# Optimization experiments

Measured on AMD Instinct MI355X. Metric: run time of the kernel, lower is better.

The kernel has to match this reference:

```python
import jax, jax.numpy as jnp
import numpy as np

EMB = 1024  # embedding_size in the torch module


def setup_inputs() -> dict:
    key = jax.random.key(0)
    ks = jax.random.split(key, 6)
    B, N, K = 64, 256, 4096
    y = jax.random.normal(ks[0], (B, N, 1024), dtype=jnp.float32)
    # nn.Linear weights, init normal(std=0.02), zero bias
    Wy_w = jax.random.normal(ks[1], (1024, 1024), dtype=jnp.float32) * 0.02  # [out,in]
    Wy_b = jnp.zeros((1024,), dtype=jnp.float32)
    Wz_w = jax.random.normal(ks[2], (1024, 2048), dtype=jnp.float32) * 0.02  # [out,in]
    Wz_b = jnp.zeros((1024,), dtype=jnp.float32)
    dic_z = jax.random.normal(ks[3], (K, 2048), dtype=jnp.float32)
    prior = jax.random.uniform(ks[4], (K,), dtype=jnp.float32)
    prior = prior / jnp.sum(prior)
    return {"y": y, "Wy_w": Wy_w, "Wy_b": Wy_b, "Wz_w": Wz_w, "Wz_b": Wz_b,
            "dic_z": dic_z, "prior": prior}


def reference(y, Wy_w, Wy_b, Wz_w, Wz_b, dic_z, prior):
    # h = Wy(y): [B,N,1024]; dz = Wz(dic_z): [K,1024]
    h = jnp.einsum('bni,oi->bno', y, Wy_w) + Wy_b
    dz = jnp.einsum('ki,oi->ko', dic_z, Wz_w) + Wz_b
    # attention over dictionary: [B,N,K]
    att = jax.nn.softmax(jnp.einsum('bnd,kd->bnk', h, dz) / jnp.sqrt(jnp.float32(EMB)), axis=-1)
    # z[b,n] = sum_k prior[k] * att[b,n,k] * dic_z[k]  -> [B,N,2048]
    # (avoids the [B,N,K,2048] intermediate the torch code materializes)
    z = jnp.einsum('bnk,k,ke->bne', att, prior, dic_z)
    return z
```

## Files before the change

kernel.cpp:

```cpp
#include <hip/hip_runtime.h>
#include <hip/hip_bf16.h>
#include <stdint.h>

typedef __bf16 bf16;
typedef __bf16 bf16x8 __attribute__((ext_vector_type(8)));
typedef float f32x4 __attribute__((ext_vector_type(4)));
typedef unsigned short ushort8 __attribute__((ext_vector_type(8)));

__device__ __forceinline__ void gload16(const bf16* g, char* l) {
  __builtin_amdgcn_global_load_lds(
      reinterpret_cast<const __attribute__((address_space(1))) unsigned int*>(
          reinterpret_cast<uintptr_t>(g)),
      reinterpret_cast<__attribute__((address_space(3))) unsigned int*>(
          reinterpret_cast<uintptr_t>(l)),
      16, 0, 0);
}

#define VMCNT(n)  asm volatile("s_waitcnt vmcnt(" #n ")" ::: "memory")
#define LGKM0()   do { asm volatile("s_waitcnt lgkmcnt(0)" ::: "memory"); \
                       __builtin_amdgcn_sched_barrier(0); } while (0)
#define BAR()     __builtin_amdgcn_s_barrier()

__global__ __launch_bounds__(256) void cast_bf16(const float* __restrict__ in,
                                                 bf16* __restrict__ out, int n8) {
  int i = blockIdx.x * blockDim.x + threadIdx.x;
  const int stride = gridDim.x * blockDim.x;
  for (; i < n8; i += stride) {
    const float4 v0 = reinterpret_cast<const float4*>(in)[i * 2];
    const float4 v1 = reinterpret_cast<const float4*>(in)[i * 2 + 1];
    bf16x8 o = { (bf16)v0.x, (bf16)v0.y, (bf16)v0.z, (bf16)v0.w,
                 (bf16)v1.x, (bf16)v1.y, (bf16)v1.z, (bf16)v1.w };
    reinterpret_cast<bf16x8*>(out)[i] = o;
  }
}

template <bool OUT_BF16, bool HAS_BIAS, int BN>
__global__ __launch_bounds__(512, 2) void gemm8(
    const bf16* __restrict__ A, const bf16* __restrict__ B,
    const float* __restrict__ bias, void* __restrict__ Cout,
    int M, int N, int K, float scale) {
  constexpr int BUFSZ = 32768 + BN * 128;
  constexpr int BOFF = 32768;
  constexpr int TM = (BN == 256) ? 128 : 64;
  constexpr int MI = TM / 16;
  constexpr int NI = 4;
  constexpr int NPH = MI / 2;
  extern __shared__ char lds[];
  const int tid = threadIdx.x;
  const int lane = tid & 63, w = tid >> 6;

  const int gridN = N / BN;
  const int nwg = gridDim.x;
  const int orig = blockIdx.x;
  int wgid;
  { const int q = nwg >> 3, r = nwg & 7, x = orig & 7, rest = orig >> 3;
    wgid = (x < r ? x * (q + 1) : r * (q + 1) + (x - r) * q) + rest; }
  const int m0 = (wgid / gridN) * 256;
  const int n0 = (wgid % gridN) * BN;

  const int srow = lane >> 3;
  const int scol = ((lane & 7) ^ srow) * 8;
  const bf16* gA = A + (size_t)(m0 + w * 8 + srow) * K + scol;
  const bf16* gB = B + (size_t)(n0 + w * 8 + srow) * K + scol;

  auto stA = [&](char* dst, int u, int h) {
    gload16(gA + (size_t)(h * 128) * K + (size_t)u * 64, dst + h * 16384 + w * 1024);
    gload16(gA + (size_t)(h * 128 + 64) * K + (size_t)u * 64, dst + h * 16384 + 8192 + w * 1024);
  };
  auto stB = [&](char* dst, int u, int h) {
    gload16(gB + (size_t)(h * 128) * K + (size_t)u * 64, dst + BOFF + h * 16384 + w * 1024);
    gload16(gB + (size_t)(h * 128 + 64) * K + (size_t)u * 64, dst + BOFF + h * 16384 + 8192 + w * 1024);
  };

  const int fr = lane & 15, hi = lane >> 4;
  int wm, wn;
  if constexpr (BN == 256) { wm = w >> 2; wn = w & 3; }
  else                     { wm = w >> 1; wn = w & 1; }
  const int abase = (wm * TM + fr) * 128 + ((hi ^ (fr & 7)) << 4);
  const int bbase = BOFF + (wn * 64 + fr) * 128 + ((hi ^ (fr & 7)) << 4);
#define RD_A(b, mi, ks) (*(const bf16x8*)((b) + ((abase + (mi) * 2048) ^ ((ks) << 6))))
#define RD_B(b, ni, ks) (*(const bf16x8*)((b) + ((bbase + (ni) * 2048) ^ ((ks) << 6))))

  f32x4 acc[MI][NI] = {};
  const int NT = K >> 6;

  stA(lds, 0, 0); stA(lds, 0, 1);
  stB(lds, 0, 0);
  if constexpr (BN == 256) stB(lds, 0, 1);
  stB(lds + BUFSZ, 1, 0);
  if constexpr (BN == 256) { stB(lds + BUFSZ, 1, 1); VMCNT(4); }
  else                     { VMCNT(2); }
  BAR();

  for (int u = 0; u < NT; ++u) {
    char* b  = lds + (size_t)(u & 1) * BUFSZ;
    char* bn = lds + (size_t)((u + 1) & 1) * BUFSZ;
    bf16x8 bb[2][NI], a[2][2];
    const bool sA = (u + 1) < NT, sB = (u + 2) < NT;

    if constexpr (BN == 256) {
      a[0][0] = RD_A(b, 0, 0); a[0][1] = RD_A(b, 0, 1);
      a[1][0] = RD_A(b, 1, 0); a[1][1] = RD_A(b, 1, 1);
#pragma unroll
      for (int ni = 0; ni < NI; ++ni) { bb[0][ni] = RD_B(b, ni, 0); bb[1][ni] = RD_B(b, ni, 1); }
      if (sA) stA(bn, u + 1, 0);
      BAR(); LGKM0();
      __builtin_amdgcn_s_setprio(1);
#pragma unroll
      for (int m2 = 0; m2 < 2; ++m2)
#pragma unroll
        for (int ni = 0; ni < NI; ++ni) {
          acc[m2][ni] = __builtin_amdgcn_mfma_f32_16x16x32_bf16(a[m2][0], bb[0][ni], acc[m2][ni], 0, 0, 0);
          acc[m2][ni] = __builtin_amdgcn_mfma_f32_16x16x32_bf16(a[m2][1], bb[1][ni], acc[m2][ni], 0, 0, 0);
        }
      __builtin_amdgcn_s_setprio(0);
      BAR();
      a[0][0] = RD_A(b, 2, 0); a[0][1] = RD_A(b, 2, 1);
      a[1][0] = RD_A(b, 3, 0); a[1][1] = RD_A(b, 3, 1);
      if (sA) stA(bn, u + 1, 1);
      BAR(); LGKM0();
      __builtin_amdgcn_s_setprio(1);
#pragma unroll
      for (int m2 = 0; m2 < 2; ++m2)
#pragma unroll
        for (int ni = 0; ni < NI; ++ni) {
          acc[2 + m2][ni] = __builtin_amdgcn_mfma_f32_16x16x32_bf16(a[m2][0], bb[0][ni], acc[2 + m2][ni], 0, 0, 0);
          acc[2 + m2][ni] = __builtin_amdgcn_mfma_f32_16x16x32_bf16(a[m2][1], bb[1][ni], acc[2 + m2][ni], 0, 0, 0);
        }
      __builtin_amdgcn_s_setprio(0);
      BAR();
      a[0][0] = RD_A(b, 4, 0); a[0][1] = RD_A(b, 4, 1);
      a[1][0] = RD_A(b, 5, 0); a[1][1] = RD_A(b, 5, 1);
      if (sB) stB(b, u + 2, 0);
      BAR(); LGKM0();
      __builtin_amdgcn_s_setprio(1);
#pragma unroll
      for (int m2 = 0; m2 < 2; ++m2)
#pragma unroll
        for (int ni = 0; ni < NI; ++ni) {
          acc[4 + m2][ni] = __builtin_amdgcn_mfma_f32_16x16x32_bf16(a[m2][0], bb[0][ni], acc[4 + m2][ni], 0, 0, 0);
          acc[4 + m2][ni] = __builtin_amdgcn_mfma_f32_16x16x32_bf16(a[m2][1], bb[1][ni], acc[4 + m2][ni], 0, 0, 0);
        }
      __builtin_amdgcn_s_setprio(0);
      BAR();
      a[0][0] = RD_A(b, 6, 0); a[0][1] = RD_A(b, 6, 1);
      a[1][0] = RD_A(b, 7, 0); a[1][1] = RD_A(b, 7, 1);
      if (sB) stB(b, u + 2, 1);
      BAR(); LGKM0();
      __builtin_amdgcn_s_setprio(1);
#pragma unroll
      for (int m2 = 0; m2 < 2; ++m2)
#pragma unroll
        for (int ni = 0; ni < NI; ++ni) {
          acc[6 + m2][ni] = __builtin_amdgcn_mfma_f32_16x16x32_bf16(a[m2][0], bb[0][ni], acc[6 + m2][ni], 0, 0, 0);
          acc[6 + m2][ni] = __builtin_amdgcn_mfma_f32_16x16x32_bf16(a[m2][1], bb[1][ni], acc[6 + m2][ni], 0, 0, 0);
        }
      __builtin_amdgcn_s_setprio(0);
      if (sB) VMCNT(4); else VMCNT(0);
      BAR();
    } else {
      a[0][0] = RD_A(b, 0, 0); a[0][1] = RD_A(b, 0, 1);
      a[1][0] = RD_A(b, 1, 0); a[1][1] = RD_A(b, 1, 1);
#pragma unroll
      for (int ni = 0; ni < NI; ++ni) { bb[0][ni] = RD_B(b, ni, 0); bb[1][ni] = RD_B(b, ni, 1); }
      if (sA) { stA(bn, u + 1, 0); stA(bn, u + 1, 1); }
      BAR(); LGKM0();
      __builtin_amdgcn_s_setprio(1);
#pragma unroll
      for (int m2 = 0; m2 < 2; ++m2)
#pragma unroll
        for (int ni = 0; ni < NI; ++ni) {
          acc[m2][ni] = __builtin_amdgcn_mfma_f32_16x16x32_bf16(a[m2][0], bb[0][ni], acc[m2][ni], 0, 0, 0);
          acc[m2][ni] = __builtin_amdgcn_mfma_f32_16x16x32_bf16(a[m2][1], bb[1][ni], acc[m2][ni], 0, 0, 0);
        }
      __builtin_amdgcn_s_setprio(0);
      BAR();
      a[0][0] = RD_A(b, 2, 0); a[0][1] = RD_A(b, 2, 1);
      a[1][0] = RD_A(b, 3, 0); a[1][1] = RD_A(b, 3, 1);
      if (sB) stB(b, u + 2, 0);
      BAR(); LGKM0();
      __builtin_amdgcn_s_setprio(1);
#pragma unroll
      for (int m2 = 0; m2 < 2; ++m2)
#pragma unroll
        for (int ni = 0; ni < NI; ++ni) {
          acc[2 + m2][ni] = __builtin_amdgcn_mfma_f32_16x16x32_bf16(a[m2][0], bb[0][ni], acc[2 + m2][ni], 0, 0, 0);
          acc[2 + m2][ni] = __builtin_amdgcn_mfma_f32_16x16x32_bf16(a[m2][1], bb[1][ni], acc[2 + m2][ni], 0, 0, 0);
        }
      __builtin_amdgcn_s_setprio(0);
      if (sB) VMCNT(2); else VMCNT(0);
      BAR();
    }
  }
#undef RD_A
#undef RD_B

  const int lro = hi * 4;
#pragma unroll
  for (int ni = 0; ni < NI; ++ni) {
    const int gcol = n0 + wn * 64 + ni * 16 + fr;
    float bvs = 0.f;
    if constexpr (HAS_BIAS) bvs = bias[gcol];
#pragma unroll
    for (int mi = 0; mi < MI; ++mi) {
      const int grow = m0 + wm * TM + mi * 16 + lro;
#pragma unroll
      for (int j = 0; j < 4; ++j) {
        const float c = acc[mi][ni][j] * scale + bvs;
        if constexpr (OUT_BF16)
          ((bf16*)Cout)[(size_t)(grow + j) * N + gcol] = (bf16)c;
        else
          ((float*)Cout)[(size_t)(grow + j) * N + gcol] = c;
      }
    }
  }
}

__global__ __launch_bounds__(256) void prep_w3t(const float* __restrict__ dic,
                                                const float* __restrict__ prior,
                                                bf16* __restrict__ w3t) {
  const int KD = 4096, E = 2048;
  __shared__ bf16 t[64][72];
  const int k0 = blockIdx.x * 64, e0 = blockIdx.y * 64;
  const int tid = threadIdx.x;
  const int er = (tid & 15) * 4;
  const int kr = tid >> 4;
#pragma unroll
  for (int p = 0; p < 4; ++p) {
    const int k = kr + p * 16;
    const float pr = prior[k0 + k];
    const float4 v = *reinterpret_cast<const float4*>(dic + (size_t)(k0 + k) * E + e0 + er);
    t[er + 0][k] = (bf16)(v.x * pr);
    t[er + 1][k] = (bf16)(v.y * pr);
    t[er + 2][k] = (bf16)(v.z * pr);
    t[er + 3][k] = (bf16)(v.w * pr);
  }
  __syncthreads();
  const int e = tid >> 2, kc = (tid & 3) * 16;
  ushort8 a = *reinterpret_cast<ushort8*>(&t[e][kc]);
  ushort8 b = *reinterpret_cast<ushort8*>(&t[e][kc + 8]);
  unsigned short* dst = (unsigned short*)w3t + (size_t)(e0 + e) * KD + k0 + kc;
  *reinterpret_cast<ushort8*>(dst) = a;
  *reinterpret_cast<ushort8*>(dst + 8) = b;
}

__global__ __launch_bounds__(256) void softmax_rows(unsigned short* __restrict__ S) {
  const int K = 4096;
  unsigned short* row = S + (size_t)blockIdx.x * K;
  const int tid = threadIdx.x;
  const int lane = tid & 63, w = tid >> 6;
  __shared__ float red[8];

  ushort8 v0 = *reinterpret_cast<const ushort8*>(row + tid * 8);
  ushort8 v1 = *reinterpret_cast<const ushort8*>(row + 2048 + tid * 8);
  float x[16];
#pragma unroll
  for (int i = 0; i < 8; ++i) {
    x[i]     = __uint_as_float(((unsigned)v0[i]) << 16);
    x[8 + i] = __uint_as_float(((unsigned)v1[i]) << 16);
  }
  float mx = x[0];
#pragma unroll
  for (int i = 1; i < 16; ++i) mx = fmaxf(mx, x[i]);
#pragma unroll
  for (int o = 32; o; o >>= 1) mx = fmaxf(mx, __shfl_xor(mx, o));
  if (lane == 0) red[w] = mx;
  __syncthreads();
  mx = fmaxf(fmaxf(red[0], red[1]), fmaxf(red[2], red[3]));

  float s = 0.f;
#pragma unroll
  for (int i = 0; i < 16; ++i) { x[i] = __expf(x[i] - mx); s += x[i]; }
#pragma unroll
  for (int o = 32; o; o >>= 1) s += __shfl_xor(s, o);
  if (lane == 0) red[4 + w] = s;
  __syncthreads();
  const float inv = 1.f / (red[4] + red[5] + red[6] + red[7]);

  ushort8 o0, o1;
#pragma unroll
  for (int i = 0; i < 8; ++i) {
    bf16 b0 = (bf16)(x[i] * inv);
    bf16 b1 = (bf16)(x[8 + i] * inv);
    o0[i] = __builtin_bit_cast(unsigned short, b0);
    o1[i] = __builtin_bit_cast(unsigned short, b1);
  }
  *reinterpret_cast<ushort8*>(row + tid * 8) = o0;
  *reinterpret_cast<ushort8*>(row + 2048 + tid * 8) = o1;
}

extern "C" void kernel_launch(void* const* d_in, const int* in_sizes, int n_in,
                              void* d_out, int out_size, void* d_ws, size_t ws_size,
                              hipStream_t stream) {
  const float* y     = (const float*)d_in[0];
  const float* Wy_w  = (const float*)d_in[1];
  const float* Wy_b  = (const float*)d_in[2];
  const float* Wz_w  = (const float*)d_in[3];
  const float* Wz_b  = (const float*)d_in[4];
  const float* dic   = (const float*)d_in[5];
  const float* prior = (const float*)d_in[6];
  float* z = (float*)d_out;

  const int M = 16384, D = 1024, E = 2048, KD = 4096;

  char* ws = (char*)d_ws;
  bf16* w3t  = (bf16*)(ws);
  bf16* h    = (bf16*)(ws + ((size_t)16 << 20));
  bf16* dzb  = (bf16*)(ws + ((size_t)48 << 20));
  bf16* S    = (bf16*)(ws + ((size_t)56 << 20));
  bf16* yb   = (bf16*)(ws + ((size_t)56 << 20));
  bf16* Wyb  = (bf16*)(ws + ((size_t)88 << 20));
  bf16* Wzb  = (bf16*)(ws + ((size_t)90 << 20));
  bf16* dicb = (bf16*)(ws + ((size_t)94 << 20));

  cast_bf16<<<2048, 256, 0, stream>>>(y, yb, M * D / 8);
  cast_bf16<<<512, 256, 0, stream>>>(Wy_w, Wyb, D * D / 8);
  cast_bf16<<<512, 256, 0, stream>>>(Wz_w, Wzb, D * E / 8);
  cast_bf16<<<1024, 256, 0, stream>>>(dic, dicb, KD * E / 8);
  prep_w3t<<<dim3(KD / 64, E / 64), 256, 0, stream>>>(dic, prior, w3t);
  gemm8<true, true, 256><<<(M / 256) * (D / 256), 512, 131072, stream>>>(
      yb, Wyb, Wy_b, h, M, D, D, 1.0f);
  gemm8<true, true, 128><<<(KD / 256) * (D / 128), 512, 98304, stream>>>(
      dicb, Wzb, Wz_b, dzb, KD, D, E, 1.0f);
  gemm8<true, false, 256><<<(M / 256) * (KD / 256), 512, 131072, stream>>>(
      h, dzb, nullptr, S, M, KD, D, 0.03125f);
  softmax_rows<<<M, 256, 0, stream>>>((unsigned short*)S);
  gemm8<false, false, 256><<<(M / 256) * (E / 256), 512, 131072, stream>>>(
      S, w3t, nullptr, z, M, E, KD, 1.0f);
}
```

Measured before the change: 562.2 us.

## Fuse softmax into GEMM epilogues and merge dic cast with weight prep

Drops the separate softmax pass. The score GEMM now writes exp(scaled score) in bf16 with no max subtraction, and the final GEMM sums the A operand per row as it streams and divides the output by that sum in its epilogue. The dictionary bf16 cast is also merged into the transposed prior-weighted prep kernel, which removes one launch and one read of dic. This saves a full read-write pass over the 16384x4096 score matrix, but skipping the max makes it vulnerable to overflow for large logits. The row sums come from bf16-rounded exp values and the extra adds run inside the MFMA loop.

```diff
diff --git a/kernel.cpp b/kernel.cpp
--- a/kernel.cpp
+++ b/kernel.cpp
@@ -3,6 +3,7 @@
 #include <stdint.h>
 
 typedef __bf16 bf16;
+typedef __bf16 bf16x4 __attribute__((ext_vector_type(4)));
 typedef __bf16 bf16x8 __attribute__((ext_vector_type(8)));
 typedef float f32x4 __attribute__((ext_vector_type(4)));
 typedef unsigned short ushort8 __attribute__((ext_vector_type(8)));
@@ -34,7 +35,7 @@
   }
 }
 
-template <bool OUT_BF16, bool HAS_BIAS, int BN>
+template <int EPI, int BN>
 __global__ __launch_bounds__(512, 2) void gemm8(
     const bf16* __restrict__ A, const bf16* __restrict__ B,
     const float* __restrict__ bias, void* __restrict__ Cout,
@@ -44,7 +45,6 @@
   constexpr int TM = (BN == 256) ? 128 : 64;
   constexpr int MI = TM / 16;
   constexpr int NI = 4;
-  constexpr int NPH = MI / 2;
   extern __shared__ char lds[];
   const int tid = threadIdx.x;
   const int lane = tid & 63, w = tid >> 6;
@@ -82,6 +82,10 @@
 #define RD_B(b, ni, ks) (*(const bf16x8*)((b) + ((bbase + (ni) * 2048) ^ ((ks) << 6))))
 
   f32x4 acc[MI][NI] = {};
+  float srowsum[MI];
+#pragma unroll
+  for (int i = 0; i < MI; ++i) srowsum[i] = 0.f;
+
   const int NT = K >> 6;
 
   stA(lds, 0, 0); stA(lds, 0, 1);
@@ -92,6 +96,13 @@
   else                     { VMCNT(2); }
   BAR();
 
+#define SUMA(Q) do { if constexpr (EPI == 2) { if (wn == 0) {                  \
+      _Pragma("unroll") for (int m2_ = 0; m2_ < 2; ++m2_)                      \
+        _Pragma("unroll") for (int ks_ = 0; ks_ < 2; ++ks_)                    \
+          _Pragma("unroll") for (int j_ = 0; j_ < 8; ++j_)                     \
+            srowsum[(Q) * 2 + m2_] += (float)a[m2_][ks_][j_];                  \
+    } } } while (0)
+
   for (int u = 0; u < NT; ++u) {
     char* b  = lds + (size_t)(u & 1) * BUFSZ;
     char* bn = lds + (size_t)((u + 1) & 1) * BUFSZ;
@@ -105,6 +116,7 @@
       for (int ni = 0; ni < NI; ++ni) { bb[0][ni] = RD_B(b, ni, 0); bb[1][ni] = RD_B(b, ni, 1); }
       if (sA) stA(bn, u + 1, 0);
       BAR(); LGKM0();
+      SUMA(0);
       __builtin_amdgcn_s_setprio(1);
 #pragma unroll
       for (int m2 = 0; m2 < 2; ++m2)
@@ -119,6 +131,7 @@
       a[1][0] = RD_A(b, 3, 0); a[1][1] = RD_A(b, 3, 1);
       if (sA) stA(bn, u + 1, 1);
       BAR(); LGKM0();
+      SUMA(1);
       __builtin_amdgcn_s_setprio(1);
 #pragma unroll
       for (int m2 = 0; m2 < 2; ++m2)
@@ -133,6 +146,7 @@
       a[1][0] = RD_A(b, 5, 0); a[1][1] = RD_A(b, 5, 1);
       if (sB) stB(b, u + 2, 0);
       BAR(); LGKM0();
+      SUMA(2);
       __builtin_amdgcn_s_setprio(1);
 #pragma unroll
       for (int m2 = 0; m2 < 2; ++m2)
@@ -147,6 +161,7 @@
       a[1][0] = RD_A(b, 7, 0); a[1][1] = RD_A(b, 7, 1);
       if (sB) stB(b, u + 2, 1);
       BAR(); LGKM0();
+      SUMA(3);
       __builtin_amdgcn_s_setprio(1);
 #pragma unroll
       for (int m2 = 0; m2 < 2; ++m2)
@@ -194,30 +209,58 @@
   }
 #undef RD_A
 #undef RD_B
-
-  const int lro = hi * 4;
-#pragma unroll
-  for (int ni = 0; ni < NI; ++ni) {
-    const int gcol = n0 + wn * 64 + ni * 16 + fr;
-    float bvs = 0.f;
-    if constexpr (HAS_BIAS) bvs = bias[gcol];
-#pragma unroll
-    for (int mi = 0; mi < MI; ++mi) {
-      const int grow = m0 + wm * TM + mi * 16 + lro;
-#pragma unroll
-      for (int j = 0; j < 4; ++j) {
-        const float c = acc[mi][ni][j] * scale + bvs;
-        if constexpr (OUT_BF16)
-          ((bf16*)Cout)[(size_t)(grow + j) * N + gcol] = (bf16)c;
-        else
-          ((float*)Cout)[(size_t)(grow + j) * N + gcol] = c;
+#undef SUMA
+
+  float* lsum = (float*)lds;
+  if constexpr (EPI == 2) {
+    if (wn == 0) {
+#pragma unroll
+      for (int mi = 0; mi < MI; ++mi) {
+        float s = srowsum[mi];
+        s += __shfl_xor(s, 16);
+        s += __shfl_xor(s, 32);
+        if (hi == 0) lsum[wm * TM + mi * 16 + fr] = s;
       }
     }
-  }
-}
-
-__global__ __launch_bounds__(256) void prep_w3t(const float* __restrict__ dic,
+    __syncthreads();
+  }
+
+  const int lro = hi * 4;
+  if constexpr (EPI == 2) {
+#pragma unroll
+    for (int mi = 0; mi < MI; ++mi)
+#pragma unroll
+      for (int j = 0; j < 4; ++j) {
+        const int lr = wm * TM + mi * 16 + lro + j;
+        const float inv = 1.0f / lsum[lr];
+        const size_t grow = (size_t)(m0 + lr) * N;
+#pragma unroll
+        for (int ni = 0; ni < NI; ++ni)
+          ((float*)Cout)[grow + n0 + wn * 64 + ni * 16 + fr] = acc[mi][ni][j] * inv;
+      }
+  } else {
+#pragma unroll
+    for (int ni = 0; ni < NI; ++ni) {
+      const int gcol = n0 + wn * 64 + ni * 16 + fr;
+      float bvs = 0.f;
+      if constexpr (EPI == 0) bvs = bias[gcol];
+#pragma unroll
+      for (int mi = 0; mi < MI; ++mi) {
+        const int grow = m0 + wm * TM + mi * 16 + lro;
+#pragma unroll
+        for (int j = 0; j < 4; ++j) {
+          float c = acc[mi][ni][j] * scale + bvs;
+          if constexpr (EPI == 1) c = __expf(c);
+          ((bf16*)Cout)[(size_t)(grow + j) * N + gcol] = (bf16)c;
+        }
+      }
+    }
+  }
+}
+
+__global__ __launch_bounds__(256) void prep_dic(const float* __restrict__ dic,
                                                 const float* __restrict__ prior,
+                                                bf16* __restrict__ dicb,
                                                 bf16* __restrict__ w3t) {
   const int KD = 4096, E = 2048;
   __shared__ bf16 t[64][72];
@@ -230,6 +273,8 @@
     const int k = kr + p * 16;
     const float pr = prior[k0 + k];
     const float4 v = *reinterpret_cast<const float4*>(dic + (size_t)(k0 + k) * E + e0 + er);
+    bf16x4 db = { (bf16)v.x, (bf16)v.y, (bf16)v.z, (bf16)v.w };
+    *reinterpret_cast<bf16x4*>(dicb + (size_t)(k0 + k) * E + e0 + er) = db;
     t[er + 0][k] = (bf16)(v.x * pr);
     t[er + 1][k] = (bf16)(v.y * pr);
     t[er + 2][k] = (bf16)(v.z * pr);
@@ -242,51 +287,6 @@
   unsigned short* dst = (unsigned short*)w3t + (size_t)(e0 + e) * KD + k0 + kc;
   *reinterpret_cast<ushort8*>(dst) = a;
   *reinterpret_cast<ushort8*>(dst + 8) = b;
-}
-
-__global__ __launch_bounds__(256) void softmax_rows(unsigned short* __restrict__ S) {
-  const int K = 4096;
-  unsigned short* row = S + (size_t)blockIdx.x * K;
-  const int tid = threadIdx.x;
-  const int lane = tid & 63, w = tid >> 6;
-  __shared__ float red[8];
-
-  ushort8 v0 = *reinterpret_cast<const ushort8*>(row + tid * 8);
-  ushort8 v1 = *reinterpret_cast<const ushort8*>(row + 2048 + tid * 8);
-  float x[16];
-#pragma unroll
-  for (int i = 0; i < 8; ++i) {
-    x[i]     = __uint_as_float(((unsigned)v0[i]) << 16);
-    x[8 + i] = __uint_as_float(((unsigned)v1[i]) << 16);
-  }
-  float mx = x[0];
-#pragma unroll
-  for (int i = 1; i < 16; ++i) mx = fmaxf(mx, x[i]);
-#pragma unroll
-  for (int o = 32; o; o >>= 1) mx = fmaxf(mx, __shfl_xor(mx, o));
-  if (lane == 0) red[w] = mx;
-  __syncthreads();
-  mx = fmaxf(fmaxf(red[0], red[1]), fmaxf(red[2], red[3]));
-
-  float s = 0.f;
-#pragma unroll
-  for (int i = 0; i < 16; ++i) { x[i] = __expf(x[i] - mx); s += x[i]; }
-#pragma unroll
-  for (int o = 32; o; o >>= 1) s += __shfl_xor(s, o);
-  if (lane == 0) red[4 + w] = s;
-  __syncthreads();
-  const float inv = 1.f / (red[4] + red[5] + red[6] + red[7]);
-
-  ushort8 o0, o1;
-#pragma unroll
-  for (int i = 0; i < 8; ++i) {
-    bf16 b0 = (bf16)(x[i] * inv);
-    bf16 b1 = (bf16)(x[8 + i] * inv);
-    o0[i] = __builtin_bit_cast(unsigned short, b0);
-    o1[i] = __builtin_bit_cast(unsigned short, b1);
-  }
-  *reinterpret_cast<ushort8*>(row + tid * 8) = o0;
-  *reinterpret_cast<ushort8*>(row + 2048 + tid * 8) = o1;
 }
 
 extern "C" void kernel_launch(void* const* d_in, const int* in_sizes, int n_in,
@@ -316,15 +316,13 @@
   cast_bf16<<<2048, 256, 0, stream>>>(y, yb, M * D / 8);
   cast_bf16<<<512, 256, 0, stream>>>(Wy_w, Wyb, D * D / 8);
   cast_bf16<<<512, 256, 0, stream>>>(Wz_w, Wzb, D * E / 8);
-  cast_bf16<<<1024, 256, 0, stream>>>(dic, dicb, KD * E / 8);
-  prep_w3t<<<dim3(KD / 64, E / 64), 256, 0, stream>>>(dic, prior, w3t);
-  gemm8<true, true, 256><<<(M / 256) * (D / 256), 512, 131072, stream>>>(
+  prep_dic<<<dim3(KD / 64, E / 64), 256, 0, stream>>>(dic, prior, dicb, w3t);
+  gemm8<0, 256><<<(M / 256) * (D / 256), 512, 131072, stream>>>(
       yb, Wyb, Wy_b, h, M, D, D, 1.0f);
-  gemm8<true, true, 128><<<(KD / 256) * (D / 128), 512, 98304, stream>>>(
+  gemm8<0, 128><<<(KD / 256) * (D / 128), 512, 98304, stream>>>(
       dicb, Wzb, Wz_b, dzb, KD, D, E, 1.0f);
-  gemm8<true, false, 256><<<(M / 256) * (KD / 256), 512, 131072, stream>>>(
+  gemm8<1, 256><<<(M / 256) * (KD / 256), 512, 131072, stream>>>(
       h, dzb, nullptr, S, M, KD, D, 0.03125f);
-  softmax_rows<<<M, 256, 0, stream>>>((unsigned short*)S);
-  gemm8<false, false, 256><<<(M / 256) * (E / 256), 512, 131072, stream>>>(
+  gemm8<2, 256><<<(M / 256) * (E / 256), 512, 131072, stream>>>(
       S, w3t, nullptr, z, M, E, KD, 1.0f);
 }
```

Measured after the change: 600.7 us. +6.8%, slower.
